# Kernel tuning notes

Hardware: AMD Instinct MI355X
Metric: run time of the kernel (lower is better)

## Reference

```python
import jax, jax.numpy as jnp
import numpy as np

N = 50000
E = 500000
NIN, NHID, NOUT = 256, 128, 64


def setup_inputs() -> dict:
    key = jax.random.key(0)
    ks = jax.random.split(key, 6)
    x = jax.random.normal(ks[0], (N, NIN), dtype=jnp.float32)
    edge_index = jax.random.randint(ks[1], (2, E), 0, N, dtype=jnp.int64)
    # GCNConv weights (glorot-ish scale) and biases
    W1 = jax.random.normal(ks[2], (NIN, NHID), dtype=jnp.float32) / np.sqrt(NIN)
    b1 = jnp.zeros((NHID,), dtype=jnp.float32)
    W2 = jax.random.normal(ks[3], (NHID, NHID), dtype=jnp.float32) / np.sqrt(NHID)
    b2 = jnp.zeros((NHID,), dtype=jnp.float32)
    # decoder Linear
    Wd = jax.random.normal(ks[4], (NHID, NOUT), dtype=jnp.float32) / np.sqrt(NHID)
    bd = jnp.zeros((NOUT,), dtype=jnp.float32)
    return {"x": x, "edge_index": edge_index, "W1": W1, "b1": b1,
            "W2": W2, "b2": b2, "Wd": Wd, "bd": bd}


def _gcn_norm(edge_index, n):
    # add self-loops, then symmetric normalization deg^-1/2 * deg^-1/2
    loops = jnp.arange(n, dtype=edge_index.dtype)
    src = jnp.concatenate([edge_index[0], loops])
    dst = jnp.concatenate([edge_index[1], loops])
    deg = jax.ops.segment_sum(jnp.ones_like(dst, dtype=jnp.float32), dst,
                              num_segments=n)
    dis = jnp.where(deg > 0, jax.lax.rsqrt(deg), 0.0)
    norm = dis[src] * dis[dst]  # [E + N]
    return src, dst, norm


def _gcn_conv(h, W, b, src, dst, norm, n):
    h = h @ W                              # [N, out]
    msg = h[src] * norm[:, None]           # gather + scale  [E+N, out]
    agg = jax.ops.segment_sum(msg, dst, num_segments=n)  # scatter-add
    return agg + b


def reference(x, edge_index, W1, b1, W2, b2, Wd, bd):
    n = x.shape[0]
    src, dst, norm = _gcn_norm(edge_index, n)
    h = jax.nn.relu(_gcn_conv(x, W1, b1, src, dst, norm, n))
    h = jax.nn.relu(_gcn_conv(h, W2, b2, src, dst, norm, n))
    # dropout is a no-op in eval mode
    out = h @ Wd + bd
    return out, h
```

## Files before the change

kernel.cpp:

```cpp
#include <hip/hip_runtime.h>

#define NIN 256
#define NHID 128
#define NOUT 64
#define CAP 64

typedef __attribute__((ext_vector_type(8))) short bf16x8;
typedef __attribute__((ext_vector_type(4))) float f32x4;

__device__ __forceinline__ unsigned int bf16_rne(float v) {
    unsigned int b = __float_as_uint(v);
    return (b + 0x7fffu + ((b >> 16) & 1u)) >> 16;
}
__device__ __forceinline__ float bf16_to_f(unsigned int bits16) {
    return __uint_as_float(bits16 << 16);
}


__global__ __launch_bounds__(256) void init_kernel(int* cursor, int n) {
    int i = blockIdx.x * 256 + threadIdx.x;
    if (i < n) cursor[i] = 0;
}

__global__ __launch_bounds__(256) void fill_bucket_kernel(const int* __restrict__ src,
                                                          const int* __restrict__ dst,
                                                          int* __restrict__ cursor,
                                                          int* __restrict__ bucket, int E) {
    int e = blockIdx.x * 256 + threadIdx.x;
    if (e >= E) return;
    int d = dst[e];
    int pos = atomicAdd(&cursor[d], 1);
    if (pos < CAP) bucket[(size_t)d * CAP + pos] = src[e];
}

__global__ __launch_bounds__(256) void dis_kernel(const int* __restrict__ cursor,
                                                  float* __restrict__ dis, int n) {
    int i = blockIdx.x * 256 + threadIdx.x;
    if (i < n) dis[i] = rsqrtf((float)(cursor[i] + 1));
}

__global__ __launch_bounds__(256) void pack_w_kernel(const float* __restrict__ W,
                                                     uint4* __restrict__ hi,
                                                     uint4* __restrict__ lo,
                                                     int K, int N) {
    int idx = blockIdx.x * 256 + threadIdx.x;
    int total = (K / 32) * (N / 16) * 64;
    if (idx >= total) return;
    int lane = idx & 63;
    int f = idx >> 6;
    int nct = N / 16;
    int ct = f % nct;
    int kt = f / nct;
    int col = ct * 16 + (lane & 15);
    int k0 = kt * 32 + (lane >> 4) * 8;
    unsigned int hs[8], ls[8];
#pragma unroll
    for (int e = 0; e < 8; ++e) {
        float v = W[(size_t)(k0 + e) * N + col];
        unsigned int h = bf16_rne(v);
        float hf = __uint_as_float(h << 16);
        ls[e] = bf16_rne(v - hf);
        hs[e] = h;
    }
    uint4 hv, lv;
    hv.x = hs[0] | (hs[1] << 16); hv.y = hs[2] | (hs[3] << 16);
    hv.z = hs[4] | (hs[5] << 16); hv.w = hs[6] | (hs[7] << 16);
    lv.x = ls[0] | (ls[1] << 16); lv.y = ls[2] | (ls[3] << 16);
    lv.z = ls[4] | (ls[5] << 16); lv.w = ls[6] | (ls[7] << 16);
    hi[idx] = hv;
    lo[idx] = lv;
}

template<int K, int NCOL, bool BIAS, bool XBF, bool OBF>
__global__ __launch_bounds__(256) void gemm_mfma_kernel(const void* __restrict__ Xv,
                                                        const uint4* __restrict__ Bhi,
                                                        const uint4* __restrict__ Blo,
                                                        const float* __restrict__ bias,
                                                        void* __restrict__ Yv, int nrows) {
    constexpr int NKT = K / 32;
    constexpr int NCT = NCOL / 16;
    __shared__ uint4 lds_b[2][NCT][64];

    int t = threadIdx.x;
    int lane = t & 63;
    int w = t >> 6;
    int row0 = blockIdx.x * 64 + w * 16;
    bool rowok = row0 < nrows;
    int arow = row0 + (lane & 15);
    int kbase = (lane >> 4) * 8;

    f32x4 acc[NCT];
#pragma unroll
    for (int c = 0; c < NCT; ++c)
#pragma unroll
        for (int r = 0; r < 4; ++r) acc[c][r] = 0.f;

    for (int kt = 0; kt < NKT; ++kt) {
        __syncthreads();
        {
            const uint4* sh = Bhi + (size_t)kt * NCT * 64;
            const uint4* sl = Blo + (size_t)kt * NCT * 64;
            uint4* dh = &lds_b[0][0][0];
            uint4* dl = &lds_b[1][0][0];
            for (int i = t; i < NCT * 64; i += 256) {
                dh[i] = sh[i];
                dl[i] = sl[i];
            }
        }
        __syncthreads();

        bf16x8 ahi, alo;
        if constexpr (XBF) {
            const unsigned short* X = (const unsigned short*)Xv;
            if (rowok)
                ahi = *(const bf16x8*)(X + (size_t)arow * K + kt * 32 + kbase);
            else
#pragma unroll
                for (int e = 0; e < 8; ++e) ahi[e] = 0;
        } else {
            const float* X = (const float*)Xv;
            float va[8];
            if (rowok) {
                const float* xp = X + (size_t)arow * K + kt * 32 + kbase;
                float4 v0 = *(const float4*)xp;
                float4 v1 = *(const float4*)(xp + 4);
                va[0] = v0.x; va[1] = v0.y; va[2] = v0.z; va[3] = v0.w;
                va[4] = v1.x; va[5] = v1.y; va[6] = v1.z; va[7] = v1.w;
            } else {
#pragma unroll
                for (int e = 0; e < 8; ++e) va[e] = 0.f;
            }
#pragma unroll
            for (int e = 0; e < 8; ++e) {
                unsigned int h = bf16_rne(va[e]);
                float hf = __uint_as_float(h << 16);
                unsigned int l = bf16_rne(va[e] - hf);
                ahi[e] = (short)h;
                alo[e] = (short)l;
            }
        }

#pragma unroll
        for (int c = 0; c < NCT; ++c) {
            bf16x8 bhi = *(const bf16x8*)&lds_b[0][c][lane];
            bf16x8 blo = *(const bf16x8*)&lds_b[1][c][lane];
            acc[c] = __builtin_amdgcn_mfma_f32_16x16x32_bf16(ahi, bhi, acc[c], 0, 0, 0);
            acc[c] = __builtin_amdgcn_mfma_f32_16x16x32_bf16(ahi, blo, acc[c], 0, 0, 0);
            if constexpr (!XBF)
                acc[c] = __builtin_amdgcn_mfma_f32_16x16x32_bf16(alo, bhi, acc[c], 0, 0, 0);
        }
    }

    if (rowok) {
        int rbase = row0 + (lane >> 4) * 4;
        int cbase = lane & 15;
#pragma unroll
        for (int c = 0; c < NCT; ++c) {
            int col = c * 16 + cbase;
            float bv = BIAS ? bias[col] : 0.f;
#pragma unroll
            for (int r = 0; r < 4; ++r) {
                float v = acc[c][r] + bv;
                if constexpr (OBF)
                    ((unsigned short*)Yv)[(size_t)(rbase + r) * NCOL + col] =
                        (unsigned short)bf16_rne(v);
                else
                    ((float*)Yv)[(size_t)(rbase + r) * NCOL + col] = v;
            }
        }
    }
}


__global__ __launch_bounds__(256) void agg_kernel(const unsigned int* __restrict__ Hb,
                                                  const int* __restrict__ cnt_arr,
                                                  const int* __restrict__ bucket,
                                                  const float* __restrict__ dis,
                                                  const float* __restrict__ bias,
                                                  unsigned int* __restrict__ Yb,
                                                  float* __restrict__ Yf, int n) {
    int node = (blockIdx.x * 256 + threadIdx.x) >> 6;
    int lane = threadIdx.x & 63;
    if (node >= n) return;

    float di = dis[node];
    unsigned int su = Hb[(size_t)node * 64 + lane];
    int c = cnt_arr[node];
    if (c > CAP) c = CAP;

    int s = 0;
    float wl = 0.f;
    if (lane < c) {
        s = bucket[(size_t)node * CAP + lane];
        wl = dis[s];
    }

    float ax[8], ay[8];
#pragma unroll
    for (int u = 0; u < 8; ++u) { ax[u] = 0.f; ay[u] = 0.f; }
    ax[0] = bf16_to_f(su & 0xffffu) * di;
    ay[0] = bf16_to_f(su >> 16) * di;

    for (int jj = 0; jj < c; jj += 8) {
        int   sv[8];
        float wv[8];
#pragma unroll
        for (int u = 0; u < 8; ++u) {
            sv[u] = __shfl(s, jj + u, 64);
            wv[u] = __shfl(wl, jj + u, 64);
        }
        unsigned int vv[8];
#pragma unroll
        for (int u = 0; u < 8; ++u)
            vv[u] = Hb[(size_t)sv[u] * 64 + lane];
#pragma unroll
        for (int u = 0; u < 8; ++u) {
            ax[u] += bf16_to_f(vv[u] & 0xffffu) * wv[u];
            ay[u] += bf16_to_f(vv[u] >> 16) * wv[u];
        }
    }

    float2 b = ((const float2*)bias)[lane];
    float rx = (((ax[0] + ax[1]) + (ax[2] + ax[3])) + ((ax[4] + ax[5]) + (ax[6] + ax[7]))) * di + b.x;
    float ry = (((ay[0] + ay[1]) + (ay[2] + ay[3])) + ((ay[4] + ay[5]) + (ay[6] + ay[7]))) * di + b.y;
    rx = fmaxf(rx, 0.f);
    ry = fmaxf(ry, 0.f);
    Yb[(size_t)node * 64 + lane] = bf16_rne(rx) | (bf16_rne(ry) << 16);
    if (Yf) {
        float2 o; o.x = rx; o.y = ry;
        ((float2*)(Yf + (size_t)node * NHID))[lane] = o;
    }
}


extern "C" void kernel_launch(void* const* d_in, const int* in_sizes, int n_in,
                              void* d_out, int out_size, void* d_ws, size_t ws_size,
                              hipStream_t stream) {
    const float* x  = (const float*)d_in[0];
    const int*   ei = (const int*)d_in[1];
    const float* W1 = (const float*)d_in[2];
    const float* b1 = (const float*)d_in[3];
    const float* W2 = (const float*)d_in[4];
    const float* b2 = (const float*)d_in[5];
    const float* Wd = (const float*)d_in[6];
    const float* bd = (const float*)d_in[7];

    int n = in_sizes[0] / NIN;
    int E = in_sizes[1] / 2;
    const int* src = ei;
    const int* dst = ei + E;

    char* ws = (char*)d_ws;
    size_t off = 0;
    auto alloc = [&](size_t bytes) -> void* {
        void* p = ws + off;
        off += (bytes + 255) & ~(size_t)255;
        return p;
    };
    int*   cursor = (int*)alloc((size_t)n * 4);
    float* dis    = (float*)alloc((size_t)n * 4);
    int*   bucket = (int*)alloc((size_t)n * CAP * 4);
    unsigned int* bufA = (unsigned int*)alloc((size_t)n * 64 * 4);
    unsigned int* h1b  = (unsigned int*)alloc((size_t)n * 64 * 4);
    unsigned int* bufB = (unsigned int*)alloc((size_t)n * 64 * 4);
    unsigned int* h2b  = (unsigned int*)alloc((size_t)n * 64 * 4);
    uint4* w1hi = (uint4*)alloc((size_t)(NIN / 32) * (NHID / 16) * 64 * 16);
    uint4* w1lo = (uint4*)alloc((size_t)(NIN / 32) * (NHID / 16) * 64 * 16);
    uint4* w2hi = (uint4*)alloc((size_t)(NHID / 32) * (NHID / 16) * 64 * 16);
    uint4* w2lo = (uint4*)alloc((size_t)(NHID / 32) * (NHID / 16) * 64 * 16);
    uint4* wdhi = (uint4*)alloc((size_t)(NHID / 32) * (NOUT / 16) * 64 * 16);
    uint4* wdlo = (uint4*)alloc((size_t)(NHID / 32) * (NOUT / 16) * 64 * 16);

    float* out  = (float*)d_out;
    float* hout = out + (size_t)n * NOUT;

    int gN = (n + 255) / 256;
    int gE = (E + 255) / 256;
    int gGemm = (n + 63) / 64;
    int gAgg = (n + 3) / 4;

    init_kernel<<<gN, 256, 0, stream>>>(cursor, n);
    fill_bucket_kernel<<<gE, 256, 0, stream>>>(src, dst, cursor, bucket, E);
    dis_kernel<<<gN, 256, 0, stream>>>(cursor, dis, n);

    pack_w_kernel<<<(NIN / 32) * (NHID / 16) * 64 / 256, 256, 0, stream>>>(W1, w1hi, w1lo, NIN, NHID);
    pack_w_kernel<<<(NHID / 32) * (NHID / 16) * 64 / 256, 256, 0, stream>>>(W2, w2hi, w2lo, NHID, NHID);
    pack_w_kernel<<<(NHID / 32) * (NOUT / 16) * 64 / 256, 256, 0, stream>>>(Wd, wdhi, wdlo, NHID, NOUT);

    gemm_mfma_kernel<NIN, NHID, false, false, true><<<gGemm, 256, 0, stream>>>(
        x, w1hi, w1lo, nullptr, bufA, n);
    agg_kernel<<<gAgg, 256, 0, stream>>>(bufA, cursor, bucket, dis, b1, h1b, nullptr, n);

    gemm_mfma_kernel<NHID, NHID, false, true, true><<<gGemm, 256, 0, stream>>>(
        h1b, w2hi, w2lo, nullptr, bufB, n);
    agg_kernel<<<gAgg, 256, 0, stream>>>(bufB, cursor, bucket, dis, b2, h2b, hout, n);

    gemm_mfma_kernel<NHID, NOUT, true, true, false><<<gGemm, 256, 0, stream>>>(
        h2b, wdhi, wdlo, bd, out, n);
}
```

Measured before the change: 136.6 us.

## Merge setup kernels and overlap edge bucketing with first GEMM

Folds the cursor zeroing and the three weight-packing kernels into a single setup launch. Runs the edge bucket fill and the layer-1 GEMM as different block ranges of one launch so the atomic scatter overlaps the MFMA work. Drops the separate degree-normalization kernel and its buffer, recomputing rsqrt of the degree inside the aggregation kernels. This cuts five launches and two dependency bubbles, at the cost of extra rsqrt and cursor gathers in both aggregation passes.

```diff
diff --git a/kernel.cpp b/kernel.cpp
--- a/kernel.cpp
+++ b/kernel.cpp
@@ -16,36 +16,9 @@
     return __uint_as_float(bits16 << 16);
 }
 
-
-__global__ __launch_bounds__(256) void init_kernel(int* cursor, int n) {
-    int i = blockIdx.x * 256 + threadIdx.x;
-    if (i < n) cursor[i] = 0;
-}
-
-__global__ __launch_bounds__(256) void fill_bucket_kernel(const int* __restrict__ src,
-                                                          const int* __restrict__ dst,
-                                                          int* __restrict__ cursor,
-                                                          int* __restrict__ bucket, int E) {
-    int e = blockIdx.x * 256 + threadIdx.x;
-    if (e >= E) return;
-    int d = dst[e];
-    int pos = atomicAdd(&cursor[d], 1);
-    if (pos < CAP) bucket[(size_t)d * CAP + pos] = src[e];
-}
-
-__global__ __launch_bounds__(256) void dis_kernel(const int* __restrict__ cursor,
-                                                  float* __restrict__ dis, int n) {
-    int i = blockIdx.x * 256 + threadIdx.x;
-    if (i < n) dis[i] = rsqrtf((float)(cursor[i] + 1));
-}
-
-__global__ __launch_bounds__(256) void pack_w_kernel(const float* __restrict__ W,
-                                                     uint4* __restrict__ hi,
-                                                     uint4* __restrict__ lo,
-                                                     int K, int N) {
-    int idx = blockIdx.x * 256 + threadIdx.x;
-    int total = (K / 32) * (N / 16) * 64;
-    if (idx >= total) return;
+__device__ __forceinline__ void pack_dev(const float* __restrict__ W,
+                                         uint4* __restrict__ hi, uint4* __restrict__ lo,
+                                         int K, int N, int idx) {
     int lane = idx & 63;
     int f = idx >> 6;
     int nct = N / 16;
@@ -69,6 +42,127 @@
     lv.z = ls[4] | (ls[5] << 16); lv.w = ls[6] | (ls[7] << 16);
     hi[idx] = hv;
     lo[idx] = lv;
+}
+
+__global__ __launch_bounds__(256) void setup_kernel(int* __restrict__ cursor,
+                                                    const float* __restrict__ W1,
+                                                    const float* __restrict__ W2,
+                                                    const float* __restrict__ Wd,
+                                                    uint4* __restrict__ w1hi, uint4* __restrict__ w1lo,
+                                                    uint4* __restrict__ w2hi, uint4* __restrict__ w2lo,
+                                                    uint4* __restrict__ wdhi, uint4* __restrict__ wdlo,
+                                                    int n, int GZ) {
+    int bid = blockIdx.x;
+    int t = threadIdx.x;
+    if (bid < GZ) {
+        int i = bid * 256 + t;
+        if (i < n) cursor[i] = 0;
+    } else {
+        int pidx = (bid - GZ) * 256 + t;
+        if (pidx < 4096)       pack_dev(W1, w1hi, w1lo, NIN,  NHID, pidx);
+        else if (pidx < 6144)  pack_dev(W2, w2hi, w2lo, NHID, NHID, pidx - 4096);
+        else                   pack_dev(Wd, wdhi, wdlo, NHID, NOUT, pidx - 6144);
+    }
+}
+
+__global__ __launch_bounds__(256) void mega_kernel(const float* __restrict__ x,
+                                                   const int* __restrict__ src,
+                                                   const int* __restrict__ dst,
+                                                   int* __restrict__ cursor,
+                                                   int* __restrict__ bucket,
+                                                   const uint4* __restrict__ Bhi,
+                                                   const uint4* __restrict__ Blo,
+                                                   unsigned int* __restrict__ bufA,
+                                                   int n, int E, int GG) {
+    constexpr int NKT = NIN / 32;
+    constexpr int NCT = NHID / 16;
+    __shared__ uint4 lds_b[2][NCT][64];
+
+    int bid = blockIdx.x;
+    int t = threadIdx.x;
+
+    if (bid >= GG) {
+        int e = (bid - GG) * 256 + t;
+        if (e < E) {
+            int d = dst[e];
+            int pos = atomicAdd(&cursor[d], 1);
+            if (pos < CAP) bucket[(size_t)d * CAP + pos] = src[e];
+        }
+        return;
+    }
+
+    int lane = t & 63;
+    int w = t >> 6;
+    int row0 = bid * 64 + w * 16;
+    bool rowok = row0 < n;
+    int arow = row0 + (lane & 15);
+    int kbase = (lane >> 4) * 8;
+
+    f32x4 acc[NCT];
+#pragma unroll
+    for (int c = 0; c < NCT; ++c)
+#pragma unroll
+        for (int r = 0; r < 4; ++r) acc[c][r] = 0.f;
+
+    for (int kt = 0; kt < NKT; ++kt) {
+        __syncthreads();
+        {
+            const uint4* sh = Bhi + (size_t)kt * NCT * 64;
+            const uint4* sl = Blo + (size_t)kt * NCT * 64;
+            uint4* dh = &lds_b[0][0][0];
+            uint4* dl = &lds_b[1][0][0];
+            for (int i = t; i < NCT * 64; i += 256) {
+                dh[i] = sh[i];
+                dl[i] = sl[i];
+            }
+        }
+        __syncthreads();
+
+        bf16x8 ahi, alo;
+        {
+            float va[8];
+            if (rowok) {
+                const float* xp = x + (size_t)arow * NIN + kt * 32 + kbase;
+                float4 v0 = *(const float4*)xp;
+                float4 v1 = *(const float4*)(xp + 4);
+                va[0] = v0.x; va[1] = v0.y; va[2] = v0.z; va[3] = v0.w;
+                va[4] = v1.x; va[5] = v1.y; va[6] = v1.z; va[7] = v1.w;
+            } else {
+#pragma unroll
+                for (int e = 0; e < 8; ++e) va[e] = 0.f;
+            }
+#pragma unroll
+            for (int e = 0; e < 8; ++e) {
+                unsigned int h = bf16_rne(va[e]);
+                float hf = __uint_as_float(h << 16);
+                unsigned int l = bf16_rne(va[e] - hf);
+                ahi[e] = (short)h;
+                alo[e] = (short)l;
+            }
+        }
+
+#pragma unroll
+        for (int c = 0; c < NCT; ++c) {
+            bf16x8 bhi = *(const bf16x8*)&lds_b[0][c][lane];
+            bf16x8 blo = *(const bf16x8*)&lds_b[1][c][lane];
+            acc[c] = __builtin_amdgcn_mfma_f32_16x16x32_bf16(ahi, bhi, acc[c], 0, 0, 0);
+            acc[c] = __builtin_amdgcn_mfma_f32_16x16x32_bf16(ahi, blo, acc[c], 0, 0, 0);
+            acc[c] = __builtin_amdgcn_mfma_f32_16x16x32_bf16(alo, bhi, acc[c], 0, 0, 0);
+        }
+    }
+
+    if (rowok) {
+        int rbase = row0 + (lane >> 4) * 4;
+        int cbase = lane & 15;
+        unsigned short* Y = (unsigned short*)bufA;
+#pragma unroll
+        for (int c = 0; c < NCT; ++c) {
+            int col = c * 16 + cbase;
+#pragma unroll
+            for (int r = 0; r < 4; ++r)
+                Y[(size_t)(rbase + r) * NHID + col] = (unsigned short)bf16_rne(acc[c][r]);
+        }
+    }
 }
 
 template<int K, int NCOL, bool BIAS, bool XBF, bool OBF>
@@ -171,11 +265,9 @@
     }
 }
 
-
 __global__ __launch_bounds__(256) void agg_kernel(const unsigned int* __restrict__ Hb,
-                                                  const int* __restrict__ cnt_arr,
+                                                  const int* __restrict__ cursor,
                                                   const int* __restrict__ bucket,
-                                                  const float* __restrict__ dis,
                                                   const float* __restrict__ bias,
                                                   unsigned int* __restrict__ Yb,
                                                   float* __restrict__ Yf, int n) {
@@ -183,16 +275,16 @@
     int lane = threadIdx.x & 63;
     if (node >= n) return;
 
-    float di = dis[node];
+    int deg = cursor[node];
+    float di = rsqrtf((float)(deg + 1));
     unsigned int su = Hb[(size_t)node * 64 + lane];
-    int c = cnt_arr[node];
-    if (c > CAP) c = CAP;
+    int c = min(deg, CAP);
 
     int s = 0;
     float wl = 0.f;
     if (lane < c) {
         s = bucket[(size_t)node * CAP + lane];
-        wl = dis[s];
+        wl = rsqrtf((float)(cursor[s] + 1));
     }
 
     float ax[8], ay[8];
@@ -258,7 +350,6 @@
         return p;
     };
     int*   cursor = (int*)alloc((size_t)n * 4);
-    float* dis    = (float*)alloc((size_t)n * 4);
     int*   bucket = (int*)alloc((size_t)n * CAP * 4);
     unsigned int* bufA = (unsigned int*)alloc((size_t)n * 64 * 4);
     unsigned int* h1b  = (unsigned int*)alloc((size_t)n * 64 * 4);
@@ -274,26 +365,23 @@
     float* out  = (float*)d_out;
     float* hout = out + (size_t)n * NOUT;
 
-    int gN = (n + 255) / 256;
-    int gE = (E + 255) / 256;
-    int gGemm = (n + 63) / 64;
+    int GZ = (n + 255) / 256;
+    int GG = (n + 63) / 64;
+    int GF = (E + 255) / 256;
+    int gGemm = GG;
     int gAgg = (n + 3) / 4;
 
-    init_kernel<<<gN, 256, 0, stream>>>(cursor, n);
-    fill_bucket_kernel<<<gE, 256, 0, stream>>>(src, dst, cursor, bucket, E);
-    dis_kernel<<<gN, 256, 0, stream>>>(cursor, dis, n);
-
-    pack_w_kernel<<<(NIN / 32) * (NHID / 16) * 64 / 256, 256, 0, stream>>>(W1, w1hi, w1lo, NIN, NHID);
-    pack_w_kernel<<<(NHID / 32) * (NHID / 16) * 64 / 256, 256, 0, stream>>>(W2, w2hi, w2lo, NHID, NHID);
-    pack_w_kernel<<<(NHID / 32) * (NOUT / 16) * 64 / 256, 256, 0, stream>>>(Wd, wdhi, wdlo, NHID, NOUT);
-
-    gemm_mfma_kernel<NIN, NHID, false, false, true><<<gGemm, 256, 0, stream>>>(
-        x, w1hi, w1lo, nullptr, bufA, n);
-    agg_kernel<<<gAgg, 256, 0, stream>>>(bufA, cursor, bucket, dis, b1, h1b, nullptr, n);
+    setup_kernel<<<GZ + 28, 256, 0, stream>>>(cursor, W1, W2, Wd,
+                                              w1hi, w1lo, w2hi, w2lo, wdhi, wdlo, n, GZ);
+
+    mega_kernel<<<GG + GF, 256, 0, stream>>>(x, src, dst, cursor, bucket,
+                                             w1hi, w1lo, bufA, n, E, GG);
+
+    agg_kernel<<<gAgg, 256, 0, stream>>>(bufA, cursor, bucket, b1, h1b, nullptr, n);
 
     gemm_mfma_kernel<NHID, NHID, false, true, true><<<gGemm, 256, 0, stream>>>(
         h1b, w2hi, w2lo, nullptr, bufB, n);
-    agg_kernel<<<gAgg, 256, 0, stream>>>(bufB, cursor, bucket, dis, b2, h2b, hout, n);
+    agg_kernel<<<gAgg, 256, 0, stream>>>(bufB, cursor, bucket, b2, h2b, hout, n);
 
     gemm_mfma_kernel<NHID, NOUT, true, true, false><<<gGemm, 256, 0, stream>>>(
         h2b, wdhi, wdlo, bd, out, n);
```

New measurement: 118.7 us. -13.1%, faster.

## Build adjacency with LDS-partitioned atomics and fuse weight packing into one kernel

Applied to the files above, without the earlier changes.

The init, bucket-fill, degree and three weight-pack launches are replaced by one kernel. In that kernel, 32 blocks each own a range of destination nodes, scan the whole edge list and count with LDS atomics. The remaining blocks pack the weights. Neighbor indices become 16-bit and degrees 8-bit, which shrinks adjacency traffic in the aggregation kernels. The cost is that each of the 32 blocks re-reads all edges with low parallelism. The code also relies on n fitting in 16 bits and on at most 1568 nodes per range.

```diff
diff --git a/kernel.cpp b/kernel.cpp
--- a/kernel.cpp
+++ b/kernel.cpp
@@ -3,7 +3,8 @@
 #define NIN 256
 #define NHID 128
 #define NOUT 64
-#define CAP 64
+#define RNG 32
+#define NPRMAX 1568
 
 typedef __attribute__((ext_vector_type(8))) short bf16x8;
 typedef __attribute__((ext_vector_type(4))) float f32x4;
@@ -16,36 +17,9 @@
     return __uint_as_float(bits16 << 16);
 }
 
-
-__global__ __launch_bounds__(256) void init_kernel(int* cursor, int n) {
-    int i = blockIdx.x * 256 + threadIdx.x;
-    if (i < n) cursor[i] = 0;
-}
-
-__global__ __launch_bounds__(256) void fill_bucket_kernel(const int* __restrict__ src,
-                                                          const int* __restrict__ dst,
-                                                          int* __restrict__ cursor,
-                                                          int* __restrict__ bucket, int E) {
-    int e = blockIdx.x * 256 + threadIdx.x;
-    if (e >= E) return;
-    int d = dst[e];
-    int pos = atomicAdd(&cursor[d], 1);
-    if (pos < CAP) bucket[(size_t)d * CAP + pos] = src[e];
-}
-
-__global__ __launch_bounds__(256) void dis_kernel(const int* __restrict__ cursor,
-                                                  float* __restrict__ dis, int n) {
-    int i = blockIdx.x * 256 + threadIdx.x;
-    if (i < n) dis[i] = rsqrtf((float)(cursor[i] + 1));
-}
-
-__global__ __launch_bounds__(256) void pack_w_kernel(const float* __restrict__ W,
-                                                     uint4* __restrict__ hi,
-                                                     uint4* __restrict__ lo,
-                                                     int K, int N) {
-    int idx = blockIdx.x * 256 + threadIdx.x;
-    int total = (K / 32) * (N / 16) * 64;
-    if (idx >= total) return;
+__device__ __forceinline__ void pack_dev(const float* __restrict__ W,
+                                         uint4* __restrict__ hi, uint4* __restrict__ lo,
+                                         int K, int N, int idx) {
     int lane = idx & 63;
     int f = idx >> 6;
     int nct = N / 16;
@@ -69,6 +43,57 @@
     lv.z = ls[4] | (ls[5] << 16); lv.w = ls[6] | (ls[7] << 16);
     hi[idx] = hv;
     lo[idx] = lv;
+}
+
+__global__ __launch_bounds__(256) void buildpack_kernel(
+        const int* __restrict__ src, const int* __restrict__ dst,
+        unsigned short* __restrict__ adj16, unsigned char* __restrict__ degc,
+        float* __restrict__ dis,
+        const float* __restrict__ W1, const float* __restrict__ W2,
+        const float* __restrict__ Wd,
+        uint4* __restrict__ w1hi, uint4* __restrict__ w1lo,
+        uint4* __restrict__ w2hi, uint4* __restrict__ w2lo,
+        uint4* __restrict__ wdhi, uint4* __restrict__ wdlo,
+        int n, int E) {
+    __shared__ int cur[NPRMAX];
+    int bid = blockIdx.x;
+    int t = threadIdx.x;
+
+    if (bid < RNG) {
+        int npr_rt = (n + RNG - 1) / RNG;
+        int base = bid * npr_rt;
+        int npr = min(npr_rt, n - base);
+        if (npr <= 0) return;
+        for (int i = t; i < npr; i += 256) cur[i] = 0;
+        __syncthreads();
+
+        for (int i = t * 4; i < E; i += 1024) {
+            int4 d4 = *(const int4*)(dst + i);
+            int4 s4 = *(const int4*)(src + i);
+            int dd[4] = {d4.x, d4.y, d4.z, d4.w};
+            int ss[4] = {s4.x, s4.y, s4.z, s4.w};
+#pragma unroll
+            for (int u = 0; u < 4; ++u) {
+                unsigned int rel = (unsigned int)(dd[u] - base);
+                if (rel < (unsigned int)npr) {
+                    int pos = atomicAdd(&cur[rel], 1);
+                    if (pos < 64)
+                        adj16[(size_t)dd[u] * 64 + pos] = (unsigned short)ss[u];
+                }
+            }
+        }
+        __syncthreads();
+        for (int i = t; i < npr; i += 256) {
+            int c = min(cur[i], 64);
+            degc[base + i] = (unsigned char)c;
+            dis[base + i] = rsqrtf((float)(c + 1));
+        }
+    } else {
+        int pidx = (bid - RNG) * 256 + t;
+        if (pidx < 4096)       pack_dev(W1, w1hi, w1lo, NIN,  NHID, pidx);
+        else if (pidx < 6144)  pack_dev(W2, w2hi, w2lo, NHID, NHID, pidx - 4096);
+        else                   pack_dev(Wd, wdhi, wdlo, NHID, NOUT, pidx - 6144);
+    }
 }
 
 template<int K, int NCOL, bool BIAS, bool XBF, bool OBF>
@@ -171,10 +196,9 @@
     }
 }
 
-
 __global__ __launch_bounds__(256) void agg_kernel(const unsigned int* __restrict__ Hb,
-                                                  const int* __restrict__ cnt_arr,
-                                                  const int* __restrict__ bucket,
+                                                  const unsigned char* __restrict__ degc,
+                                                  const unsigned short* __restrict__ adj16,
                                                   const float* __restrict__ dis,
                                                   const float* __restrict__ bias,
                                                   unsigned int* __restrict__ Yb,
@@ -183,15 +207,14 @@
     int lane = threadIdx.x & 63;
     if (node >= n) return;
 
+    int cnt = (int)degc[node];
     float di = dis[node];
     unsigned int su = Hb[(size_t)node * 64 + lane];
-    int c = cnt_arr[node];
-    if (c > CAP) c = CAP;
 
     int s = 0;
     float wl = 0.f;
-    if (lane < c) {
-        s = bucket[(size_t)node * CAP + lane];
+    if (lane < cnt) {
+        s = (int)adj16[(size_t)node * 64 + lane];
         wl = dis[s];
     }
 
@@ -201,7 +224,7 @@
     ax[0] = bf16_to_f(su & 0xffffu) * di;
     ay[0] = bf16_to_f(su >> 16) * di;
 
-    for (int jj = 0; jj < c; jj += 8) {
+    for (int jj = 0; jj < cnt; jj += 8) {
         int   sv[8];
         float wv[8];
 #pragma unroll
@@ -257,9 +280,9 @@
         off += (bytes + 255) & ~(size_t)255;
         return p;
     };
-    int*   cursor = (int*)alloc((size_t)n * 4);
-    float* dis    = (float*)alloc((size_t)n * 4);
-    int*   bucket = (int*)alloc((size_t)n * CAP * 4);
+    unsigned short* adj16 = (unsigned short*)alloc((size_t)n * 64 * 2);
+    unsigned char* degc   = (unsigned char*)alloc((size_t)n);
+    float* dis            = (float*)alloc((size_t)n * 4);
     unsigned int* bufA = (unsigned int*)alloc((size_t)n * 64 * 4);
     unsigned int* h1b  = (unsigned int*)alloc((size_t)n * 64 * 4);
     unsigned int* bufB = (unsigned int*)alloc((size_t)n * 64 * 4);
@@ -274,27 +297,22 @@
     float* out  = (float*)d_out;
     float* hout = out + (size_t)n * NOUT;
 
-    int gN = (n + 255) / 256;
-    int gE = (E + 255) / 256;
-    int gGemm = (n + 63) / 64;
+    int GG = (n + 63) / 64;
     int gAgg = (n + 3) / 4;
 
-    init_kernel<<<gN, 256, 0, stream>>>(cursor, n);
-    fill_bucket_kernel<<<gE, 256, 0, stream>>>(src, dst, cursor, bucket, E);
-    dis_kernel<<<gN, 256, 0, stream>>>(cursor, dis, n);
-
-    pack_w_kernel<<<(NIN / 32) * (NHID / 16) * 64 / 256, 256, 0, stream>>>(W1, w1hi, w1lo, NIN, NHID);
-    pack_w_kernel<<<(NHID / 32) * (NHID / 16) * 64 / 256, 256, 0, stream>>>(W2, w2hi, w2lo, NHID, NHID);
-    pack_w_kernel<<<(NHID / 32) * (NOUT / 16) * 64 / 256, 256, 0, stream>>>(Wd, wdhi, wdlo, NHID, NOUT);
-
-    gemm_mfma_kernel<NIN, NHID, false, false, true><<<gGemm, 256, 0, stream>>>(
+    buildpack_kernel<<<RNG + 28, 256, 0, stream>>>(
+        src, dst, adj16, degc, dis, W1, W2, Wd,
+        w1hi, w1lo, w2hi, w2lo, wdhi, wdlo, n, E);
+
+    gemm_mfma_kernel<NIN, NHID, false, false, true><<<GG, 256, 0, stream>>>(
         x, w1hi, w1lo, nullptr, bufA, n);
-    agg_kernel<<<gAgg, 256, 0, stream>>>(bufA, cursor, bucket, dis, b1, h1b, nullptr, n);
-
-    gemm_mfma_kernel<NHID, NHID, false, true, true><<<gGemm, 256, 0, stream>>>(
+
+    agg_kernel<<<gAgg, 256, 0, stream>>>(bufA, degc, adj16, dis, b1, h1b, nullptr, n);
+
+    gemm_mfma_kernel<NHID, NHID, false, true, true><<<GG, 256, 0, stream>>>(
         h1b, w2hi, w2lo, nullptr, bufB, n);
-    agg_kernel<<<gAgg, 256, 0, stream>>>(bufB, cursor, bucket, dis, b2, h2b, hout, n);
-
-    gemm_mfma_kernel<NHID, NOUT, true, true, false><<<gGemm, 256, 0, stream>>>(
+    agg_kernel<<<gAgg, 256, 0, stream>>>(bufB, degc, adj16, dis, b2, h2b, hout, n);
+
+    gemm_mfma_kernel<NHID, NOUT, true, true, false><<<GG, 256, 0, stream>>>(
         h2b, wdhi, wdlo, bd, out, n);
 }
```

Result: slower. 414.0 us (+203.0%).
